# Performance work log

Measured on AMD Instinct MI355X. Metric: run time of the kernel, lower is better.

## Reference

```python
import jax, jax.numpy as jnp
import numpy as np

TEMP = 0.1
EPS = 1e-8  # torch cosine_similarity eps
B, P, N, D = 256, 32, 512, 256


def setup_inputs() -> dict:
    key = jax.random.key(0)
    k1, k2, k3 = jax.random.split(key, 3)
    return {
        "anchors": jax.random.normal(k1, (B, D), dtype=jnp.float32),
        "positives": jax.random.normal(k2, (B, P, D), dtype=jnp.float32),
        "negatives": jax.random.normal(k3, (B, N, D), dtype=jnp.float32),
    }


def reference(anchors, positives, negatives):
    # all_samples: (B, K, D) with K = P + N
    all_samples = jnp.concatenate([positives, negatives], axis=1)
    # Cosine similarity of anchor vs every sample (the original broadcasts the
    # anchor over P identical rows; we compute the (B, K) row once).
    dots = jnp.einsum("bd,bkd->bk", anchors, all_samples)          # (B, K)
    na = jnp.linalg.norm(anchors, axis=-1, keepdims=True)           # (B, 1)
    nk = jnp.linalg.norm(all_samples, axis=-1)                      # (B, K)
    sim = dots / jnp.maximum(na * nk, EPS) / TEMP                   # (B, K)
    logp = jax.nn.log_softmax(sim, axis=-1)                         # (B, K)
    p = positives.shape[1]
    # labels = arange(P): gather picks -log_softmax at column p for row p;
    # since all P rows equal, this is just the first P columns of logp.
    return -jnp.mean(logp[:, :p])
```

## Files before the change

### kernel.cpp

```cpp
#include <hip/hip_runtime.h>
#include <math.h>

#define TEMP_INV 10.0f
#define EPS 1e-8f
#define B_ 256
#define P_ 32
#define N_ 512
#define D_ 256
#define K_ (P_ + N_)
#define G_ (K_ / 4)

__device__ __forceinline__ float wave_reduce_sum(float v) {
    #pragma unroll
    for (int m = 32; m >= 1; m >>= 1) v += __shfl_xor(v, m, 64);
    return v;
}

__device__ __forceinline__ float wave_reduce_max(float v) {
    #pragma unroll
    for (int m = 32; m >= 1; m >>= 1) v = fmaxf(v, __shfl_xor(v, m, 64));
    return v;
}

__device__ __forceinline__ float dot4(float4 a, float4 b) {
    return a.x * b.x + a.y * b.y + a.z * b.z + a.w * b.w;
}

__global__ __launch_bounds__(256) void sim_kernel(
    const float* __restrict__ anchors,
    const float* __restrict__ positives,
    const float* __restrict__ negatives,
    float* __restrict__ sim,
    float* __restrict__ out) {
    int gw   = blockIdx.x * 4 + (threadIdx.x >> 6);
    int lane = threadIdx.x & 63;
    int b  = gw / G_;
    int g  = gw - b * G_;
    int k0 = g * 4;

    const float4* a4 = (const float4*)(anchors + (size_t)b * D_);
    float4 a = a4[lane];

    const float4* base = (k0 < P_)
        ? (const float4*)(positives + ((size_t)b * P_ + k0) * D_)
        : (const float4*)(negatives + ((size_t)b * N_ + (k0 - P_)) * D_);

    float4 s0 = base[lane];
    float4 s1 = base[64 + lane];
    float4 s2 = base[128 + lane];
    float4 s3 = base[192 + lane];

    float na = sqrtf(wave_reduce_sum(dot4(a, a)));

    float d0 = wave_reduce_sum(dot4(a, s0));
    float q0 = wave_reduce_sum(dot4(s0, s0));
    float d1 = wave_reduce_sum(dot4(a, s1));
    float q1 = wave_reduce_sum(dot4(s1, s1));
    float d2 = wave_reduce_sum(dot4(a, s2));
    float q2 = wave_reduce_sum(dot4(s2, s2));
    float d3 = wave_reduce_sum(dot4(a, s3));
    float q3 = wave_reduce_sum(dot4(s3, s3));

    if (lane == 0) {
        float* row = sim + (size_t)b * K_ + k0;
        row[0] = d0 / fmaxf(na * sqrtf(q0), EPS) * TEMP_INV;
        row[1] = d1 / fmaxf(na * sqrtf(q1), EPS) * TEMP_INV;
        row[2] = d2 / fmaxf(na * sqrtf(q2), EPS) * TEMP_INV;
        row[3] = d3 / fmaxf(na * sqrtf(q3), EPS) * TEMP_INV;
    }

    if (blockIdx.x == 0 && threadIdx.x == 0) out[0] = 0.0f;
}

__global__ __launch_bounds__(256) void softmax_kernel(
    const float* __restrict__ sim,
    float* __restrict__ out) {
    int b    = blockIdx.x;
    int tid  = threadIdx.x;
    int wid  = tid >> 6;
    int lane = tid & 63;
    const float* row = sim + (size_t)b * K_;

    float vals[3];
    int cnt = 0;
    float lmax = -INFINITY;
    for (int k = tid; k < K_; k += 256) {
        float v = row[k];
        vals[cnt++] = v;
        lmax = fmaxf(lmax, v);
    }

    __shared__ float s_max[4];
    __shared__ float s_sum[4];
    __shared__ float s_pos[4];

    float wmax = wave_reduce_max(lmax);
    if (lane == 0) s_max[wid] = wmax;
    __syncthreads();
    float bmax = fmaxf(fmaxf(s_max[0], s_max[1]), fmaxf(s_max[2], s_max[3]));

    float lsum = 0.0f;
    for (int i = 0; i < cnt; i++) lsum += expf(vals[i] - bmax);
    float wsum = wave_reduce_sum(lsum);
    if (lane == 0) s_sum[wid] = wsum;

    float lp = (tid < P_) ? vals[0] : 0.0f;
    float wp = wave_reduce_sum(lp);
    if (lane == 0) s_pos[wid] = wp;
    __syncthreads();

    if (tid == 0) {
        float bsum = s_sum[0] + s_sum[1] + s_sum[2] + s_sum[3];
        float bpos = s_pos[0] + s_pos[1] + s_pos[2] + s_pos[3];
        float lse  = bmax + logf(bsum);
        float partial = ((float)P_ * lse - bpos) * (1.0f / (float)(B_ * P_));
        atomicAdd(out, partial);
    }
}

extern "C" void kernel_launch(void* const* d_in, const int* in_sizes, int n_in,
                              void* d_out, int out_size, void* d_ws, size_t ws_size,
                              hipStream_t stream) {
    const float* anchors   = (const float*)d_in[0];
    const float* positives = (const float*)d_in[1];
    const float* negatives = (const float*)d_in[2];
    float* out = (float*)d_out;
    float* sim = (float*)d_ws;

    int n_waves  = B_ * G_;
    int n_blocks = n_waves / 4;
    sim_kernel<<<n_blocks, 256, 0, stream>>>(anchors, positives, negatives, sim, out);
    softmax_kernel<<<B_, 256, 0, stream>>>(sim, out);
}
```

Baseline: 201.8 us.

## Fuse exp-sum into similarity pass with fixed max and 8-lane row reductions

The similarity kernel now assigns 16 sample rows to each wave, with 8 lanes per row. This cuts each row's dot-product and norm reductions to 3 shuffles instead of full 64-lane wave reductions. Because cosine similarity divided by the temperature is bounded by 10, the log-sum-exp uses that constant as its max. Exponentials and positive sums are accumulated per chunk, so the similarity matrix never needs to be written out. A single-block finalize kernel replaces the per-row softmax kernel and its atomic, at the cost of a serial sum over 34 chunk partials per row.

```diff
diff --git a/kernel.cpp b/kernel.cpp
--- a/kernel.cpp
+++ b/kernel.cpp
@@ -8,114 +8,112 @@
 #define N_ 512
 #define D_ 256
 #define K_ (P_ + N_)
-#define G_ (K_ / 4)
-
-__device__ __forceinline__ float wave_reduce_sum(float v) {
-    #pragma unroll
-    for (int m = 32; m >= 1; m >>= 1) v += __shfl_xor(v, m, 64);
-    return v;
-}
-
-__device__ __forceinline__ float wave_reduce_max(float v) {
-    #pragma unroll
-    for (int m = 32; m >= 1; m >>= 1) v = fmaxf(v, __shfl_xor(v, m, 64));
-    return v;
-}
+#define CHUNK_ 16
+#define NCHUNK_ (K_ / CHUNK_)
 
 __device__ __forceinline__ float dot4(float4 a, float4 b) {
     return a.x * b.x + a.y * b.y + a.z * b.z + a.w * b.w;
 }
 
-__global__ __launch_bounds__(256) void sim_kernel(
+__device__ __forceinline__ float reduce_sub8(float v) {
+    v += __shfl_xor(v, 1, 64);
+    v += __shfl_xor(v, 2, 64);
+    v += __shfl_xor(v, 4, 64);
+    return v;
+}
+
+__device__ __forceinline__ float reduce_grp8(float v) {
+    v += __shfl_xor(v, 8, 64);
+    v += __shfl_xor(v, 16, 64);
+    v += __shfl_xor(v, 32, 64);
+    return v;
+}
+
+__global__ __launch_bounds__(256) void partial_kernel(
     const float* __restrict__ anchors,
     const float* __restrict__ positives,
     const float* __restrict__ negatives,
-    float* __restrict__ sim,
-    float* __restrict__ out) {
+    float* __restrict__ S_ws,
+    float* __restrict__ POS_ws)
+{
+    int lane = threadIdx.x & 63;
     int gw   = blockIdx.x * 4 + (threadIdx.x >> 6);
-    int lane = threadIdx.x & 63;
-    int b  = gw / G_;
-    int g  = gw - b * G_;
-    int k0 = g * 4;
+    int b = gw / NCHUNK_;
+    int c = gw - b * NCHUNK_;
+    int sub = lane & 7;
+    int jj  = lane >> 3;
 
     const float4* a4 = (const float4*)(anchors + (size_t)b * D_);
-    float4 a = a4[lane];
+    float4 a[8];
+    #pragma unroll
+    for (int p = 0; p < 8; p++) a[p] = a4[p * 8 + sub];
 
-    const float4* base = (k0 < P_)
-        ? (const float4*)(positives + ((size_t)b * P_ + k0) * D_)
-        : (const float4*)(negatives + ((size_t)b * N_ + (k0 - P_)) * D_);
+    int k0 = c * CHUNK_;
+    const float* base = (k0 < P_)
+        ? positives + ((size_t)b * P_ + k0) * D_
+        : negatives + ((size_t)b * N_ + (k0 - P_)) * D_;
 
-    float4 s0 = base[lane];
-    float4 s1 = base[64 + lane];
-    float4 s2 = base[128 + lane];
-    float4 s3 = base[192 + lane];
+    float napart = 0.f;
+    #pragma unroll
+    for (int p = 0; p < 8; p++) napart += dot4(a[p], a[p]);
+    float na = sqrtf(reduce_sub8(napart));
 
-    float na = sqrtf(wave_reduce_sum(dot4(a, a)));
+    float e_acc = 0.f;
+    float p_acc = 0.f;
 
-    float d0 = wave_reduce_sum(dot4(a, s0));
-    float q0 = wave_reduce_sum(dot4(s0, s0));
-    float d1 = wave_reduce_sum(dot4(a, s1));
-    float q1 = wave_reduce_sum(dot4(s1, s1));
-    float d2 = wave_reduce_sum(dot4(a, s2));
-    float q2 = wave_reduce_sum(dot4(s2, s2));
-    float d3 = wave_reduce_sum(dot4(a, s3));
-    float q3 = wave_reduce_sum(dot4(s3, s3));
+    #pragma unroll
+    for (int t = 0; t < 2; t++) {
+        const float4* r = (const float4*)(base + (size_t)(t * 8 + jj) * D_);
+        float4 s[8];
+        #pragma unroll
+        for (int p = 0; p < 8; p++) s[p] = r[p * 8 + sub];
 
-    if (lane == 0) {
-        float* row = sim + (size_t)b * K_ + k0;
-        row[0] = d0 / fmaxf(na * sqrtf(q0), EPS) * TEMP_INV;
-        row[1] = d1 / fmaxf(na * sqrtf(q1), EPS) * TEMP_INV;
-        row[2] = d2 / fmaxf(na * sqrtf(q2), EPS) * TEMP_INV;
-        row[3] = d3 / fmaxf(na * sqrtf(q3), EPS) * TEMP_INV;
+        float dpart = 0.f, qpart = 0.f;
+        #pragma unroll
+        for (int p = 0; p < 8; p++) {
+            dpart += dot4(a[p], s[p]);
+            qpart += dot4(s[p], s[p]);
+        }
+        float dj = reduce_sub8(dpart);
+        float qj = reduce_sub8(qpart);
+
+        float sim = dj / fmaxf(na * sqrtf(qj), EPS) * TEMP_INV;
+        e_acc += expf(sim - 10.0f);
+        p_acc += sim;
     }
 
-    if (blockIdx.x == 0 && threadIdx.x == 0) out[0] = 0.0f;
+    e_acc = reduce_grp8(e_acc);
+    if (lane == 0) S_ws[c * B_ + b] = e_acc;
+
+    if (c < 2) {
+        float ps = reduce_grp8(p_acc);
+        if (lane == 0) POS_ws[c * B_ + b] = ps;
+    }
 }
 
-__global__ __launch_bounds__(256) void softmax_kernel(
-    const float* __restrict__ sim,
-    float* __restrict__ out) {
-    int b    = blockIdx.x;
-    int tid  = threadIdx.x;
-    int wid  = tid >> 6;
-    int lane = tid & 63;
-    const float* row = sim + (size_t)b * K_;
+__global__ __launch_bounds__(256) void finalize_kernel(
+    const float* __restrict__ S_ws,
+    const float* __restrict__ POS_ws,
+    float* __restrict__ out)
+{
+    int t    = threadIdx.x;
+    int wid  = t >> 6;
+    int lane = t & 63;
 
-    float vals[3];
-    int cnt = 0;
-    float lmax = -INFINITY;
-    for (int k = tid; k < K_; k += 256) {
-        float v = row[k];
-        vals[cnt++] = v;
-        lmax = fmaxf(lmax, v);
-    }
+    float s = 0.f;
+    #pragma unroll
+    for (int i = 0; i < NCHUNK_; i++) s += S_ws[i * B_ + t];
+    float v  = logf(s);
+    float pp = POS_ws[t] + POS_ws[B_ + t];
 
-    __shared__ float s_max[4];
-    __shared__ float s_sum[4];
-    __shared__ float s_pos[4];
+    float red = v * (1.0f / (float)B_) - pp * (1.0f / (float)(B_ * P_));
+    #pragma unroll
+    for (int m = 32; m >= 1; m >>= 1) red += __shfl_xor(red, m, 64);
 
-    float wmax = wave_reduce_max(lmax);
-    if (lane == 0) s_max[wid] = wmax;
+    __shared__ float sh[4];
+    if (lane == 0) sh[wid] = red;
     __syncthreads();
-    float bmax = fmaxf(fmaxf(s_max[0], s_max[1]), fmaxf(s_max[2], s_max[3]));
-
-    float lsum = 0.0f;
-    for (int i = 0; i < cnt; i++) lsum += expf(vals[i] - bmax);
-    float wsum = wave_reduce_sum(lsum);
-    if (lane == 0) s_sum[wid] = wsum;
-
-    float lp = (tid < P_) ? vals[0] : 0.0f;
-    float wp = wave_reduce_sum(lp);
-    if (lane == 0) s_pos[wid] = wp;
-    __syncthreads();
-
-    if (tid == 0) {
-        float bsum = s_sum[0] + s_sum[1] + s_sum[2] + s_sum[3];
-        float bpos = s_pos[0] + s_pos[1] + s_pos[2] + s_pos[3];
-        float lse  = bmax + logf(bsum);
-        float partial = ((float)P_ * lse - bpos) * (1.0f / (float)(B_ * P_));
-        atomicAdd(out, partial);
-    }
+    if (t == 0) out[0] = 10.0f + (sh[0] + sh[1] + sh[2] + sh[3]);
 }
 
 extern "C" void kernel_launch(void* const* d_in, const int* in_sizes, int n_in,
@@ -125,10 +123,13 @@
     const float* positives = (const float*)d_in[1];
     const float* negatives = (const float*)d_in[2];
     float* out = (float*)d_out;
-    float* sim = (float*)d_ws;
 
-    int n_waves  = B_ * G_;
+    float* S_ws   = (float*)d_ws;
+    float* POS_ws = S_ws + NCHUNK_ * B_;
+
+    int n_waves  = B_ * NCHUNK_;
     int n_blocks = n_waves / 4;
-    sim_kernel<<<n_blocks, 256, 0, stream>>>(anchors, positives, negatives, sim, out);
-    softmax_kernel<<<B_, 256, 0, stream>>>(sim, out);
+    partial_kernel<<<n_blocks, 256, 0, stream>>>(anchors, positives, negatives,
+                                                 S_ws, POS_ws);
+    finalize_kernel<<<1, 256, 0, stream>>>(S_ws, POS_ws, out);
 }
```

Result: no change. 203.2 us (+0.7%).
